# Kernel tuning notes

Measured on AMD Instinct MI355X. Metric: run time of the kernel, lower is better.

The kernel has to match this reference:

```python
import jax, jax.numpy as jnp
import numpy as np

B, L, D, NH = 16, 1024, 1024, 8


def setup_inputs() -> dict:
    key = jax.random.key(0)
    k = jax.random.split(key, 5)
    return {
        "x": jax.random.normal(k[0], (B, L, D), dtype=jnp.float32),
        # last head's Conv1d(length, length, 1) weight [out_ch=L, in_ch=L] and bias [L]
        "conv_w": jax.random.normal(k[1], (L, L), dtype=jnp.float32) * 0.02,
        "conv_b": jax.random.normal(k[2], (L,), dtype=jnp.float32) * 0.02,
        # out_proj: Linear(dim*n_heads, dim) -> weight [D, D*NH], bias [D]
        "out_w": jax.random.normal(k[3], (D, D * NH), dtype=jnp.float32) * 0.02,
        "out_b": jax.random.normal(k[4], (D,), dtype=jnp.float32) * 0.02,
    }


def reference(x, conv_w, conv_b, out_w, out_b):
    # Faithful to the original (including its stale-loop-variable bug: every
    # head applies convs[-1], so the concat is NH identical copies).
    # Causal-masked softmax of the token-mixing weights. Note: torch code does
    # softmax(tril(W)) WITHOUT -inf masking, so upper-triangular zeros still
    # contribute exp(0)=1 to the softmax denominator -- reproduced exactly.
    W = jax.nn.softmax(jnp.tril(conv_w), axis=-1)          # [L, L]
    # Conv1d(kernel=1) over channel axis == token mixing: y[b,f,m] = sum_d W[f,d] x[b,d,m] + b[f]
    y = jnp.einsum('fd,bdm->bfm', W, x) + conv_b[None, :, None]  # [B, L, D]
    # concat of NH identical copies then out_proj == matmul with head-summed out_w
    w_eff = out_w.reshape(D, NH, D).sum(axis=1)            # [D, D]
    return jnp.einsum('blm,om->blo', y, w_eff) + out_b      # [B, L, D]
```

## Files before the change

### kernel.cpp

```cpp
#include <hip/hip_runtime.h>
#include <cstdint>

#define LL 1024
#define DD 1024
#define NB 16
#define NHH 8

typedef __bf16 bf16x8 __attribute__((ext_vector_type(8)));
typedef float f32x4 __attribute__((ext_vector_type(4)));
typedef unsigned short u16;

#define GPTR(x) ((const __attribute__((address_space(1))) void*)(x))
#define LPTR(x) ((__attribute__((address_space(3))) void*)(x))
#define BAR()   __builtin_amdgcn_s_barrier()
#define LGKM0() asm volatile("s_waitcnt lgkmcnt(0)" ::: "memory")
#define VMC(N)  asm volatile("s_waitcnt vmcnt(" #N ")" ::: "memory")

static __device__ __forceinline__ u16 f2b(float f) {
  unsigned int u = __float_as_uint(f);
  u += 0x7FFFu + ((u >> 16) & 1u);
  return (u16)(u >> 16);
}

__global__ __launch_bounds__(256) void prep_kernel(const float* __restrict__ x,
                                                   const float* __restrict__ conv_w,
                                                   const float* __restrict__ out_w,
                                                   u16* __restrict__ xb,
                                                   u16* __restrict__ Wb,
                                                   u16* __restrict__ weff,
                                                   float* __restrict__ S) {
  const int blk = blockIdx.x;
  const int t = threadIdx.x;
  __shared__ float red[256];

  if (blk < 1024) {
    const int o = blk;
    const float4* row = (const float4*)(out_w + (size_t)o * (DD * NHH));
    float4 s4 = {0.f, 0.f, 0.f, 0.f};
#pragma unroll
    for (int h = 0; h < NHH; ++h) {
      float4 v = row[h * 256 + t];
      s4.x += v.x; s4.y += v.y; s4.z += v.z; s4.w += v.w;
    }
    ushort4 p;
    p.x = f2b(s4.x); p.y = f2b(s4.y); p.z = f2b(s4.z); p.w = f2b(s4.w);
    *(ushort4*)&weff[(size_t)o * DD + t * 4] = p;
    red[t] = s4.x + s4.y + s4.z + s4.w;
    __syncthreads();
    for (int st = 128; st > 0; st >>= 1) {
      if (t < st) red[t] += red[t + st];
      __syncthreads();
    }
    if (t == 0) S[o] = red[0];
  } else if (blk < 2048) {
    const int f = blk - 1024;
    float z[4];
    float mx = -1e30f;
#pragma unroll
    for (int i = 0; i < 4; ++i) {
      int d = t + i * 256;
      float v = conv_w[(size_t)f * LL + d];
      z[i] = (d <= f) ? v : 0.f;
      mx = fmaxf(mx, z[i]);
    }
    red[t] = mx;
    __syncthreads();
    for (int st = 128; st > 0; st >>= 1) {
      if (t < st) red[t] = fmaxf(red[t], red[t + st]);
      __syncthreads();
    }
    mx = red[0];
    __syncthreads();
    float e[4], s = 0.f;
#pragma unroll
    for (int i = 0; i < 4; ++i) { e[i] = expf(z[i] - mx); s += e[i]; }
    red[t] = s;
    __syncthreads();
    for (int st = 128; st > 0; st >>= 1) {
      if (t < st) red[t] += red[t + st];
      __syncthreads();
    }
    float inv = 1.f / red[0];
#pragma unroll
    for (int i = 0; i < 4; ++i) Wb[(size_t)f * LL + t + i * 256] = f2b(e[i] * inv);
  } else {
    const int n8 = (NB * LL * DD) / 8;
    int i = (blk - 2048) * 256 + t;
    const int stride = 2048 * 256;
    for (; i < n8; i += stride) {
      float4 v0 = ((const float4*)x)[2 * i];
      float4 v1 = ((const float4*)x)[2 * i + 1];
      uint4 p;
      p.x = (unsigned)f2b(v0.x) | ((unsigned)f2b(v0.y) << 16);
      p.y = (unsigned)f2b(v0.z) | ((unsigned)f2b(v0.w) << 16);
      p.z = (unsigned)f2b(v1.x) | ((unsigned)f2b(v1.y) << 16);
      p.w = (unsigned)f2b(v1.z) | ((unsigned)f2b(v1.w) << 16);
      ((uint4*)xb)[i] = p;
    }
  }
}

__device__ __forceinline__ void stageTile(const u16* __restrict__ g, u16* l,
                                          int wave, int lane) {
  const int rlo = lane >> 3;
  const int sl = (lane & 7) ^ rlo;
#pragma unroll
  for (int j = 0; j < 4; ++j) {
    const u16* src = g + (size_t)(j * 64 + wave * 8 + rlo) * 1024 + sl * 8;
    __builtin_amdgcn_global_load_lds(GPTR(src), LPTR(l + j * 4096 + wave * 512), 16, 0, 0);
  }
}

__device__ __forceinline__ bf16x8 ldsRead(const u16* l, int row, int slot) {
  int off = row * 64 + (((slot) ^ (row & 7)) << 3);
  return __builtin_bit_cast(bf16x8, *(const uint4*)(l + off));
}

template <int EPI>
__global__ __launch_bounds__(512, 2) void gemm8(const u16* __restrict__ A,
                                                const u16* __restrict__ Bm,
                                                void* __restrict__ Cout,
                                                const float* __restrict__ conv_b,
                                                const float* __restrict__ S,
                                                const float* __restrict__ out_b) {
  extern __shared__ u16 lds[];
  u16* A0 = lds;
  u16* B0 = lds + 16384;
  u16* A1 = lds + 32768;
  u16* B1 = lds + 49152;

  int bid = blockIdx.x;
  bid = (bid & 7) * 32 + (bid >> 3);
  const int b = bid >> 4;
  const int tm = (bid >> 2) & 3;
  const int tn = bid & 3;

  const int tid = threadIdx.x, lane = tid & 63, wave = tid >> 6;
  const int wm = wave >> 2, wn = wave & 3;
  const int lrow = lane & 15, kg = lane >> 4;

  const u16* Ablk = A + (size_t)(tm * 256) * 1024;
  const u16* Bblk = Bm + (size_t)b * (1024 * 1024) + (size_t)(tn * 256) * 1024;

  f32x4 acc[8][4];
#pragma unroll
  for (int i = 0; i < 8; ++i)
#pragma unroll
    for (int j = 0; j < 4; ++j) acc[i][j] = (f32x4){0.f, 0.f, 0.f, 0.f};

  bf16x8 af[8], b0r[4], b1r[4];

  auto readAfr = [&](const u16* Ab, int mh) {
#pragma unroll
    for (int q = 0; q < 4; ++q)
#pragma unroll
      for (int ks = 0; ks < 2; ++ks)
        af[q * 2 + ks] = ldsRead(Ab, wm * 128 + (mh * 4 + q) * 16 + lrow, kg + 4 * ks);
  };
  auto readBfr = [&](const u16* Bb, int nh, bf16x8* dst) {
#pragma unroll
    for (int n = 0; n < 2; ++n)
#pragma unroll
      for (int ks = 0; ks < 2; ++ks)
        dst[n * 2 + ks] = ldsRead(Bb, wn * 64 + (nh * 2 + n) * 16 + lrow, kg + 4 * ks);
  };
  auto mfmaQuad = [&](int mh, int nh, bf16x8* bfr) {
    __builtin_amdgcn_s_setprio(1);
#pragma unroll
    for (int q = 0; q < 4; ++q)
#pragma unroll
      for (int n = 0; n < 2; ++n)
#pragma unroll
        for (int ks = 0; ks < 2; ++ks)
          acc[mh * 4 + q][nh * 2 + n] = __builtin_amdgcn_mfma_f32_16x16x32_bf16(
              af[q * 2 + ks], bfr[n * 2 + ks], acc[mh * 4 + q][nh * 2 + n], 0, 0, 0);
    __builtin_amdgcn_s_setprio(0);
  };

  stageTile(Ablk, A0, wave, lane);
  stageTile(Bblk, B0, wave, lane);
  stageTile(Ablk + 64, A1, wave, lane);
  stageTile(Bblk + 64, B1, wave, lane);
  VMC(8);
  BAR();

  for (int i = 0; i < 7; ++i) {
    const int t2 = 2 * i + 2, t3 = 2 * i + 3;
    readAfr(A0, 0); readBfr(B0, 0, b0r); BAR(); LGKM0(); mfmaQuad(0, 0, b0r); BAR();
    readBfr(B0, 1, b1r);                 BAR(); LGKM0(); mfmaQuad(0, 1, b1r); BAR();
    readAfr(A0, 1);                      BAR(); LGKM0(); mfmaQuad(1, 1, b1r); BAR();
    stageTile(Ablk + t2 * 64, A0, wave, lane);
    stageTile(Bblk + t2 * 64, B0, wave, lane);
    mfmaQuad(1, 0, b0r); VMC(8); BAR();
    readAfr(A1, 0); readBfr(B1, 0, b0r); BAR(); LGKM0(); mfmaQuad(0, 0, b0r); BAR();
    readBfr(B1, 1, b1r);                 BAR(); LGKM0(); mfmaQuad(0, 1, b1r); BAR();
    readAfr(A1, 1);                      BAR(); LGKM0(); mfmaQuad(1, 1, b1r); BAR();
    stageTile(Ablk + t3 * 64, A1, wave, lane);
    stageTile(Bblk + t3 * 64, B1, wave, lane);
    mfmaQuad(1, 0, b0r); VMC(8); BAR();
  }
  readAfr(A0, 0); readBfr(B0, 0, b0r); BAR(); LGKM0(); mfmaQuad(0, 0, b0r); BAR();
  readBfr(B0, 1, b1r);                 BAR(); LGKM0(); mfmaQuad(0, 1, b1r); BAR();
  readAfr(A0, 1);                      BAR(); LGKM0(); mfmaQuad(1, 1, b1r); BAR();
  mfmaQuad(1, 0, b0r); VMC(0); BAR();
  readAfr(A1, 0); readBfr(B1, 0, b0r); BAR(); LGKM0(); mfmaQuad(0, 0, b0r); BAR();
  readBfr(B1, 1, b1r);                 BAR(); LGKM0(); mfmaQuad(0, 1, b1r); BAR();
  readAfr(A1, 1);                      BAR(); LGKM0(); mfmaQuad(1, 1, b1r); BAR();
  mfmaQuad(1, 0, b0r);

  BAR();

  if constexpr (EPI == 0) {
    u16* E = lds;
#pragma unroll
    for (int mi = 0; mi < 8; ++mi)
#pragma unroll
      for (int ni = 0; ni < 4; ++ni)
#pragma unroll
        for (int j = 0; j < 4; ++j) {
          int r = wm * 128 + mi * 16 + kg * 4 + j;
          int c = wn * 64 + ni * 16 + lrow;
          E[r * 256 + (c ^ (((r >> 2) & 3) << 4))] = f2b(acc[mi][ni][j]);
        }
    __syncthreads();
    u16* Cb = (u16*)Cout + (size_t)b * (1024 * 1024) + (size_t)(tm * 256) * 1024 + tn * 256;
#pragma unroll
    for (int i = 0; i < 16; ++i) {
      int r = i * 16 + (tid >> 5);
      int cl = (tid & 31) * 8;
      uint4 v = *(const uint4*)&E[r * 256 + (cl ^ (((r >> 2) & 3) << 4))];
      *(uint4*)&Cb[(size_t)r * 1024 + cl] = v;
    }
  } else {
    float* Ef = (float*)lds;
    float* Cf = (float*)Cout + (size_t)b * (1024 * 1024) + (size_t)(tm * 256) * 1024 + tn * 256;
#pragma unroll
    for (int h = 0; h < 2; ++h) {
      if (h) __syncthreads();
#pragma unroll
      for (int mi2 = 0; mi2 < 4; ++mi2) {
        int mi = 4 * h + mi2;
#pragma unroll
        for (int ni = 0; ni < 4; ++ni) {
          int c = wn * 64 + ni * 16 + lrow;
          float sc = S[tn * 256 + c], ob = out_b[tn * 256 + c];
#pragma unroll
          for (int j = 0; j < 4; ++j) {
            int li = wm * 64 + mi2 * 16 + kg * 4 + j;
            int rg = tm * 256 + wm * 128 + mi * 16 + kg * 4 + j;
            Ef[li * 256 + (c ^ ((li & 4) << 2))] = acc[mi][ni][j] + conv_b[rg] * sc + ob;
          }
        }
      }
      __syncthreads();
#pragma unroll
      for (int i = 0; i < 16; ++i) {
        int li = i * 8 + (tid >> 6);
        int cl = (tid & 63) * 4;
        float4 v = *(const float4*)&Ef[li * 256 + (cl ^ ((li & 4) << 2))];
        int rblk = (li >> 6) * 128 + h * 64 + (li & 63);
        *(float4*)&Cf[(size_t)rblk * 1024 + cl] = v;
      }
    }
  }
}

__global__ __launch_bounds__(256) void gemmA_f32(const u16* __restrict__ weff,
                                                 const float* __restrict__ x,
                                                 u16* __restrict__ Zt) {
  __shared__ u16 Al[128 * 32];
  __shared__ u16 Bl[128 * 32];
  const int b = blockIdx.y;
  const int tid = threadIdx.x, lane = tid & 63, wave = tid >> 6;
  const int wm = wave >> 1, wn = wave & 1;
  const int tm = blockIdx.x >> 3, tn = blockIdx.x & 7;
  const int lrow = lane & 15, kg = lane >> 4;
  const float* xbp = x + (size_t)b * LL * DD;
  f32x4 acc[4][4];
#pragma unroll
  for (int i = 0; i < 4; ++i)
#pragma unroll
    for (int j = 0; j < 4; ++j) acc[i][j] = (f32x4){0.f, 0.f, 0.f, 0.f};
  const int brow = tid >> 2, bcol = (tid & 3) * 8;
  const int arow = lane >> 2, acol = (lane & 3) * 8;
  for (int k0 = 0; k0 < DD; k0 += 32) {
#pragma unroll
    for (int cc = 0; cc < 2; ++cc) {
      int c = 2 * wave + cc;
      const u16* g = weff + (size_t)(tm * 128 + c * 16 + arow) * DD + k0 + acol;
      __builtin_amdgcn_global_load_lds(GPTR(g), LPTR(Al + c * 512), 16, 0, 0);
    }
#pragma unroll
    for (int ch = 0; ch < 2; ++ch) {
      const float* gp = xbp + (size_t)(tn * 128 + ch * 64 + brow) * DD + k0 + bcol;
      float4 v0 = *(const float4*)gp;
      float4 v1 = *(const float4*)(gp + 4);
      uint4 p;
      p.x = (unsigned)f2b(v0.x) | ((unsigned)f2b(v0.y) << 16);
      p.y = (unsigned)f2b(v0.z) | ((unsigned)f2b(v0.w) << 16);
      p.z = (unsigned)f2b(v1.x) | ((unsigned)f2b(v1.y) << 16);
      p.w = (unsigned)f2b(v1.z) | ((unsigned)f2b(v1.w) << 16);
      *(uint4*)&Bl[(ch * 64 + brow) * 32 + bcol] = p;
    }
    __syncthreads();
    bf16x8 a2[4], b2[4];
#pragma unroll
    for (int mi = 0; mi < 4; ++mi)
      a2[mi] = __builtin_bit_cast(bf16x8, *(const uint4*)&Al[(wm * 64 + mi * 16 + lrow) * 32 + kg * 8]);
#pragma unroll
    for (int ni = 0; ni < 4; ++ni)
      b2[ni] = __builtin_bit_cast(bf16x8, *(const uint4*)&Bl[(wn * 64 + ni * 16 + lrow) * 32 + kg * 8]);
#pragma unroll
    for (int mi = 0; mi < 4; ++mi)
#pragma unroll
      for (int ni = 0; ni < 4; ++ni)
        acc[mi][ni] = __builtin_amdgcn_mfma_f32_16x16x32_bf16(a2[mi], b2[ni], acc[mi][ni], 0, 0, 0);
    __syncthreads();
  }
  u16* Zb = Zt + (size_t)b * DD * LL;
#pragma unroll
  for (int mi = 0; mi < 4; ++mi)
#pragma unroll
    for (int ni = 0; ni < 4; ++ni)
#pragma unroll
      for (int j = 0; j < 4; ++j) {
        int r = tm * 128 + wm * 64 + mi * 16 + kg * 4 + j;
        int c = tn * 128 + wn * 64 + ni * 16 + lrow;
        Zb[(size_t)r * LL + c] = f2b(acc[mi][ni][j]);
      }
}

__global__ __launch_bounds__(256) void gemmB2(const u16* __restrict__ Wm,
                                              const u16* __restrict__ Zt,
                                              const float* __restrict__ conv_b,
                                              const float* __restrict__ S,
                                              const float* __restrict__ out_b,
                                              float* __restrict__ out) {
  __shared__ u16 Al[128 * 32];
  __shared__ u16 Bl[128 * 32];
  const int b = blockIdx.y;
  const int tid = threadIdx.x, lane = tid & 63, wave = tid >> 6;
  const int wm = wave >> 1, wn = wave & 1;
  const int tm = blockIdx.x >> 3, tn = blockIdx.x & 7;
  const int lrow = lane & 15, kg = lane >> 4;
  const u16* Zb = Zt + (size_t)b * DD * LL;
  f32x4 acc[4][4];
#pragma unroll
  for (int i = 0; i < 4; ++i)
#pragma unroll
    for (int j = 0; j < 4; ++j) acc[i][j] = (f32x4){0.f, 0.f, 0.f, 0.f};
  const int arow = lane >> 2, acol = (lane & 3) * 8;
  for (int k0 = 0; k0 < LL; k0 += 32) {
#pragma unroll
    for (int cc = 0; cc < 2; ++cc) {
      int c = 2 * wave + cc;
      const u16* ga = Wm + (size_t)(tm * 128 + c * 16 + arow) * LL + k0 + acol;
      __builtin_amdgcn_global_load_lds(GPTR(ga), LPTR(Al + c * 512), 16, 0, 0);
      const u16* gb = Zb + (size_t)(tn * 128 + c * 16 + arow) * LL + k0 + acol;
      __builtin_amdgcn_global_load_lds(GPTR(gb), LPTR(Bl + c * 512), 16, 0, 0);
    }
    __syncthreads();
    bf16x8 a2[4], b2[4];
#pragma unroll
    for (int mi = 0; mi < 4; ++mi)
      a2[mi] = __builtin_bit_cast(bf16x8, *(const uint4*)&Al[(wm * 64 + mi * 16 + lrow) * 32 + kg * 8]);
#pragma unroll
    for (int ni = 0; ni < 4; ++ni)
      b2[ni] = __builtin_bit_cast(bf16x8, *(const uint4*)&Bl[(wn * 64 + ni * 16 + lrow) * 32 + kg * 8]);
#pragma unroll
    for (int mi = 0; mi < 4; ++mi)
#pragma unroll
      for (int ni = 0; ni < 4; ++ni)
        acc[mi][ni] = __builtin_amdgcn_mfma_f32_16x16x32_bf16(a2[mi], b2[ni], acc[mi][ni], 0, 0, 0);
    __syncthreads();
  }
#pragma unroll
  for (int ni = 0; ni < 4; ++ni) {
    int c = tn * 128 + wn * 64 + ni * 16 + lrow;
    float sc = S[c], ob = out_b[c];
#pragma unroll
    for (int mi = 0; mi < 4; ++mi)
#pragma unroll
      for (int j = 0; j < 4; ++j) {
        int r = tm * 128 + wm * 64 + mi * 16 + kg * 4 + j;
        out[((size_t)b * LL + r) * DD + c] = acc[mi][ni][j] + conv_b[r] * sc + ob;
      }
  }
}

extern "C" void kernel_launch(void* const* d_in, const int* in_sizes, int n_in,
                              void* d_out, int out_size, void* d_ws, size_t ws_size,
                              hipStream_t stream) {
  const float* x      = (const float*)d_in[0];
  const float* conv_w = (const float*)d_in[1];
  const float* conv_b = (const float*)d_in[2];
  const float* out_w  = (const float*)d_in[3];
  const float* out_b  = (const float*)d_in[4];
  float* out = (float*)d_out;

  char* ws = (char*)d_ws;
  u16*   W_bf = (u16*)ws;
  u16*   weff = (u16*)(ws + (2u << 20));
  float* S    = (float*)(ws + (4u << 20));
  u16*   Zt   = (u16*)(ws + (4u << 20) + (1u << 16));
  u16*   x_bf = (u16*)(ws + (36u << 20) + (1u << 16));
  const size_t need = (68ull << 20) + (1u << 16);

  hipError_t e0 = hipFuncSetAttribute(reinterpret_cast<const void*>(gemm8<0>),
                                      hipFuncAttributeMaxDynamicSharedMemorySize, 131072);
  hipError_t e1 = hipFuncSetAttribute(reinterpret_cast<const void*>(gemm8<1>),
                                      hipFuncAttributeMaxDynamicSharedMemorySize, 131072);
  const bool use8 = (e0 == hipSuccess) && (e1 == hipSuccess) && (ws_size >= need);

  if (use8) {
    hipLaunchKernelGGL(prep_kernel, dim3(4096), dim3(256), 0, stream,
                       x, conv_w, out_w, x_bf, W_bf, weff, S);
    hipLaunchKernelGGL((gemm8<0>), dim3(256), dim3(512), 131072, stream,
                       weff, x_bf, (void*)Zt, (const float*)nullptr,
                       (const float*)nullptr, (const float*)nullptr);
    hipLaunchKernelGGL((gemm8<1>), dim3(256), dim3(512), 131072, stream,
                       W_bf, Zt, (void*)out, conv_b, S, out_b);
  } else {
    hipLaunchKernelGGL(prep_kernel, dim3(2048), dim3(256), 0, stream,
                       x, conv_w, out_w, x_bf, W_bf, weff, S);
    hipLaunchKernelGGL(gemmA_f32, dim3(64, NB), dim3(256), 0, stream, weff, x, Zt);
    hipLaunchKernelGGL(gemmB2, dim3(64, NB), dim3(256), 0, stream, W_bf, Zt, conv_b, S, out_b, out);
  }
}
```

Before: 100.3 us.

## Use 16-wave 1024-thread GEMM blocks with smaller per-wave tiles

The 256x256 GEMM tile is now split across 16 waves (1024 threads) instead of 8, so each wave owns a 64x64 sub-tile and keeps half as many accumulators. Staging, LDS fragment reads, the MFMA schedule and both epilogues are reworked to match the new wave layout. The aim is more latency hiding and lower register pressure per wave. The cost is more barrier participants, a higher ratio of LDS reads to MFMAs per wave, and a launch-bounds hint of 4 that cannot be met with 128KB of LDS per block.

```diff
diff --git a/kernel.cpp b/kernel.cpp
--- a/kernel.cpp
+++ b/kernel.cpp
@@ -100,14 +100,14 @@
   }
 }
 
-__device__ __forceinline__ void stageTile(const u16* __restrict__ g, u16* l,
-                                          int wave, int lane) {
+__device__ __forceinline__ void stageTile16(const u16* __restrict__ g, u16* l,
+                                            int wave, int lane) {
   const int rlo = lane >> 3;
   const int sl = (lane & 7) ^ rlo;
 #pragma unroll
-  for (int j = 0; j < 4; ++j) {
-    const u16* src = g + (size_t)(j * 64 + wave * 8 + rlo) * 1024 + sl * 8;
-    __builtin_amdgcn_global_load_lds(GPTR(src), LPTR(l + j * 4096 + wave * 512), 16, 0, 0);
+  for (int j = 0; j < 2; ++j) {
+    const u16* src = g + (size_t)(j * 128 + wave * 8 + rlo) * 1024 + sl * 8;
+    __builtin_amdgcn_global_load_lds(GPTR(src), LPTR(l + j * 8192 + wave * 512), 16, 0, 0);
   }
 }
 
@@ -117,12 +117,12 @@
 }
 
 template <int EPI>
-__global__ __launch_bounds__(512, 2) void gemm8(const u16* __restrict__ A,
-                                                const u16* __restrict__ Bm,
-                                                void* __restrict__ Cout,
-                                                const float* __restrict__ conv_b,
-                                                const float* __restrict__ S,
-                                                const float* __restrict__ out_b) {
+__global__ __launch_bounds__(1024, 4) void gemm16(const u16* __restrict__ A,
+                                                  const u16* __restrict__ Bm,
+                                                  void* __restrict__ Cout,
+                                                  const float* __restrict__ conv_b,
+                                                  const float* __restrict__ S,
+                                                  const float* __restrict__ out_b) {
   extern __shared__ u16 lds[];
   u16* A0 = lds;
   u16* B0 = lds + 16384;
@@ -142,91 +142,79 @@
   const u16* Ablk = A + (size_t)(tm * 256) * 1024;
   const u16* Bblk = Bm + (size_t)b * (1024 * 1024) + (size_t)(tn * 256) * 1024;
 
-  f32x4 acc[8][4];
-#pragma unroll
-  for (int i = 0; i < 8; ++i)
+  f32x4 acc[4][4];
+#pragma unroll
+  for (int i = 0; i < 4; ++i)
 #pragma unroll
     for (int j = 0; j < 4; ++j) acc[i][j] = (f32x4){0.f, 0.f, 0.f, 0.f};
 
-  bf16x8 af[8], b0r[4], b1r[4];
-
-  auto readAfr = [&](const u16* Ab, int mh) {
+  bf16x8 af[4], bf[4];
+
+  auto readA = [&](const u16* Ab, int ks) {
 #pragma unroll
     for (int q = 0; q < 4; ++q)
-#pragma unroll
-      for (int ks = 0; ks < 2; ++ks)
-        af[q * 2 + ks] = ldsRead(Ab, wm * 128 + (mh * 4 + q) * 16 + lrow, kg + 4 * ks);
+      af[q] = ldsRead(Ab, wm * 64 + q * 16 + lrow, kg + 4 * ks);
   };
-  auto readBfr = [&](const u16* Bb, int nh, bf16x8* dst) {
-#pragma unroll
-    for (int n = 0; n < 2; ++n)
-#pragma unroll
-      for (int ks = 0; ks < 2; ++ks)
-        dst[n * 2 + ks] = ldsRead(Bb, wn * 64 + (nh * 2 + n) * 16 + lrow, kg + 4 * ks);
+  auto readB = [&](const u16* Bb, int ks) {
+#pragma unroll
+    for (int n = 0; n < 4; ++n)
+      bf[n] = ldsRead(Bb, wn * 64 + n * 16 + lrow, kg + 4 * ks);
   };
-  auto mfmaQuad = [&](int mh, int nh, bf16x8* bfr) {
+  auto mfmaN = [&](int n0, int nn) {
     __builtin_amdgcn_s_setprio(1);
 #pragma unroll
     for (int q = 0; q < 4; ++q)
 #pragma unroll
-      for (int n = 0; n < 2; ++n)
-#pragma unroll
-        for (int ks = 0; ks < 2; ++ks)
-          acc[mh * 4 + q][nh * 2 + n] = __builtin_amdgcn_mfma_f32_16x16x32_bf16(
-              af[q * 2 + ks], bfr[n * 2 + ks], acc[mh * 4 + q][nh * 2 + n], 0, 0, 0);
+      for (int n = 0; n < 4; ++n)
+        if (n >= n0 && n < n0 + nn)
+          acc[q][n] = __builtin_amdgcn_mfma_f32_16x16x32_bf16(af[q], bf[n], acc[q][n], 0, 0, 0);
     __builtin_amdgcn_s_setprio(0);
   };
 
-  stageTile(Ablk, A0, wave, lane);
-  stageTile(Bblk, B0, wave, lane);
-  stageTile(Ablk + 64, A1, wave, lane);
-  stageTile(Bblk + 64, B1, wave, lane);
-  VMC(8);
+  stageTile16(Ablk, A0, wave, lane);
+  stageTile16(Bblk, B0, wave, lane);
+  stageTile16(Ablk + 64, A1, wave, lane);
+  stageTile16(Bblk + 64, B1, wave, lane);
+  VMC(4);
   BAR();
 
   for (int i = 0; i < 7; ++i) {
     const int t2 = 2 * i + 2, t3 = 2 * i + 3;
-    readAfr(A0, 0); readBfr(B0, 0, b0r); BAR(); LGKM0(); mfmaQuad(0, 0, b0r); BAR();
-    readBfr(B0, 1, b1r);                 BAR(); LGKM0(); mfmaQuad(0, 1, b1r); BAR();
-    readAfr(A0, 1);                      BAR(); LGKM0(); mfmaQuad(1, 1, b1r); BAR();
-    stageTile(Ablk + t2 * 64, A0, wave, lane);
-    stageTile(Bblk + t2 * 64, B0, wave, lane);
-    mfmaQuad(1, 0, b0r); VMC(8); BAR();
-    readAfr(A1, 0); readBfr(B1, 0, b0r); BAR(); LGKM0(); mfmaQuad(0, 0, b0r); BAR();
-    readBfr(B1, 1, b1r);                 BAR(); LGKM0(); mfmaQuad(0, 1, b1r); BAR();
-    readAfr(A1, 1);                      BAR(); LGKM0(); mfmaQuad(1, 1, b1r); BAR();
-    stageTile(Ablk + t3 * 64, A1, wave, lane);
-    stageTile(Bblk + t3 * 64, B1, wave, lane);
-    mfmaQuad(1, 0, b0r); VMC(8); BAR();
-  }
-  readAfr(A0, 0); readBfr(B0, 0, b0r); BAR(); LGKM0(); mfmaQuad(0, 0, b0r); BAR();
-  readBfr(B0, 1, b1r);                 BAR(); LGKM0(); mfmaQuad(0, 1, b1r); BAR();
-  readAfr(A0, 1);                      BAR(); LGKM0(); mfmaQuad(1, 1, b1r); BAR();
-  mfmaQuad(1, 0, b0r); VMC(0); BAR();
-  readAfr(A1, 0); readBfr(B1, 0, b0r); BAR(); LGKM0(); mfmaQuad(0, 0, b0r); BAR();
-  readBfr(B1, 1, b1r);                 BAR(); LGKM0(); mfmaQuad(0, 1, b1r); BAR();
-  readAfr(A1, 1);                      BAR(); LGKM0(); mfmaQuad(1, 1, b1r); BAR();
-  mfmaQuad(1, 0, b0r);
+    readA(A0, 0); readB(B0, 0); BAR(); LGKM0(); mfmaN(0, 4); BAR();
+    readA(A0, 1); readB(B0, 1); BAR(); LGKM0(); mfmaN(0, 2); BAR();
+    stageTile16(Ablk + t2 * 64, A0, wave, lane);
+    stageTile16(Bblk + t2 * 64, B0, wave, lane);
+    mfmaN(2, 2); VMC(4); BAR();
+    readA(A1, 0); readB(B1, 0); BAR(); LGKM0(); mfmaN(0, 4); BAR();
+    readA(A1, 1); readB(B1, 1); BAR(); LGKM0(); mfmaN(0, 2); BAR();
+    stageTile16(Ablk + t3 * 64, A1, wave, lane);
+    stageTile16(Bblk + t3 * 64, B1, wave, lane);
+    mfmaN(2, 2); VMC(4); BAR();
+  }
+  readA(A0, 0); readB(B0, 0); BAR(); LGKM0(); mfmaN(0, 4); BAR();
+  readA(A0, 1); readB(B0, 1); BAR(); LGKM0(); mfmaN(0, 4); VMC(0); BAR();
+  readA(A1, 0); readB(B1, 0); BAR(); LGKM0(); mfmaN(0, 4); BAR();
+  readA(A1, 1); readB(B1, 1); BAR(); LGKM0(); mfmaN(0, 4);
 
   BAR();
 
   if constexpr (EPI == 0) {
     u16* E = lds;
 #pragma unroll
-    for (int mi = 0; mi < 8; ++mi)
-#pragma unroll
-      for (int ni = 0; ni < 4; ++ni)
+    for (int q = 0; q < 4; ++q)
+#pragma unroll
+      for (int n = 0; n < 4; ++n)
 #pragma unroll
         for (int j = 0; j < 4; ++j) {
-          int r = wm * 128 + mi * 16 + kg * 4 + j;
-          int c = wn * 64 + ni * 16 + lrow;
-          E[r * 256 + (c ^ (((r >> 2) & 3) << 4))] = f2b(acc[mi][ni][j]);
+          int r = wm * 64 + q * 16 + kg * 4 + j;
+          int c = wn * 64 + n * 16 + lrow;
+          E[r * 256 + (c ^ (((r >> 2) & 3) << 4))] = f2b(acc[q][n][j]);
         }
     __syncthreads();
     u16* Cb = (u16*)Cout + (size_t)b * (1024 * 1024) + (size_t)(tm * 256) * 1024 + tn * 256;
 #pragma unroll
-    for (int i = 0; i < 16; ++i) {
-      int r = i * 16 + (tid >> 5);
+    for (int i = 0; i < 8; ++i) {
+      int r = i * 32 + (tid >> 5);
       int cl = (tid & 31) * 8;
       uint4 v = *(const uint4*)&E[r * 256 + (cl ^ (((r >> 2) & 3) << 4))];
       *(uint4*)&Cb[(size_t)r * 1024 + cl] = v;
@@ -238,28 +226,31 @@
     for (int h = 0; h < 2; ++h) {
       if (h) __syncthreads();
 #pragma unroll
-      for (int mi2 = 0; mi2 < 4; ++mi2) {
-        int mi = 4 * h + mi2;
-#pragma unroll
-        for (int ni = 0; ni < 4; ++ni) {
-          int c = wn * 64 + ni * 16 + lrow;
+      for (int q2 = 0; q2 < 2; ++q2) {
+        int q = 2 * h + q2;
+#pragma unroll
+        for (int n = 0; n < 4; ++n) {
+          int c = wn * 64 + n * 16 + lrow;
           float sc = S[tn * 256 + c], ob = out_b[tn * 256 + c];
 #pragma unroll
           for (int j = 0; j < 4; ++j) {
-            int li = wm * 64 + mi2 * 16 + kg * 4 + j;
-            int rg = tm * 256 + wm * 128 + mi * 16 + kg * 4 + j;
-            Ef[li * 256 + (c ^ ((li & 4) << 2))] = acc[mi][ni][j] + conv_b[rg] * sc + ob;
+            int li = wm * 32 + q2 * 16 + kg * 4 + j;
+            int rg = tm * 256 + wm * 64 + q * 16 + kg * 4 + j;
+            Ef[li * 256 + (c ^ ((li & 4) << 2))] = acc[q][n][j] + conv_b[rg] * sc + ob;
           }
         }
       }
       __syncthreads();
 #pragma unroll
-      for (int i = 0; i < 16; ++i) {
-        int li = i * 8 + (tid >> 6);
-        int cl = (tid & 63) * 4;
-        float4 v = *(const float4*)&Ef[li * 256 + (cl ^ ((li & 4) << 2))];
-        int rblk = (li >> 6) * 128 + h * 64 + (li & 63);
-        *(float4*)&Cf[(size_t)rblk * 1024 + cl] = v;
+      for (int i = 0; i < 4; ++i) {
+        int li = i * 32 + (tid >> 5);
+        int cl = (tid & 31) * 8;
+        int cs = cl ^ ((li & 4) << 2);
+        float4 v0 = *(const float4*)&Ef[li * 256 + cs];
+        float4 v1 = *(const float4*)&Ef[li * 256 + cs + 4];
+        int r = (li >> 5) * 64 + h * 32 + (li & 31);
+        *(float4*)&Cf[(size_t)r * 1024 + cl] = v0;
+        *(float4*)&Cf[(size_t)r * 1024 + cl + 4] = v1;
       }
     }
   }
@@ -406,19 +397,19 @@
   u16*   x_bf = (u16*)(ws + (36u << 20) + (1u << 16));
   const size_t need = (68ull << 20) + (1u << 16);
 
-  hipError_t e0 = hipFuncSetAttribute(reinterpret_cast<const void*>(gemm8<0>),
+  hipError_t e0 = hipFuncSetAttribute(reinterpret_cast<const void*>(gemm16<0>),
                                       hipFuncAttributeMaxDynamicSharedMemorySize, 131072);
-  hipError_t e1 = hipFuncSetAttribute(reinterpret_cast<const void*>(gemm8<1>),
+  hipError_t e1 = hipFuncSetAttribute(reinterpret_cast<const void*>(gemm16<1>),
                                       hipFuncAttributeMaxDynamicSharedMemorySize, 131072);
-  const bool use8 = (e0 == hipSuccess) && (e1 == hipSuccess) && (ws_size >= need);
-
-  if (use8) {
+  const bool use16 = (e0 == hipSuccess) && (e1 == hipSuccess) && (ws_size >= need);
+
+  if (use16) {
     hipLaunchKernelGGL(prep_kernel, dim3(4096), dim3(256), 0, stream,
                        x, conv_w, out_w, x_bf, W_bf, weff, S);
-    hipLaunchKernelGGL((gemm8<0>), dim3(256), dim3(512), 131072, stream,
+    hipLaunchKernelGGL((gemm16<0>), dim3(256), dim3(1024), 131072, stream,
                        weff, x_bf, (void*)Zt, (const float*)nullptr,
                        (const float*)nullptr, (const float*)nullptr);
-    hipLaunchKernelGGL((gemm8<1>), dim3(256), dim3(512), 131072, stream,
+    hipLaunchKernelGGL((gemm16<1>), dim3(256), dim3(1024), 131072, stream,
                        W_bf, Zt, (void*)out, conv_b, S, out_b);
   } else {
     hipLaunchKernelGGL(prep_kernel, dim3(2048), dim3(256), 0, stream,
```

Result: slower. 113.7 us (+13.3%).
